# Optimization experiments

Hardware: AMD Instinct MI355X
Metric: run time of the kernel (lower is better)

Reference implementation:

```python
import jax, jax.numpy as jnp
import numpy as np

IN = (16, 16, 16)
OUT = (16, 16, 16)
RT = (8, 8, 8, 8, 8, 8)
RCP = 16
BATCH = 4096


def setup_inputs() -> dict:
    key = jax.random.key(0)
    ks = jax.random.split(key, 14)
    inp = {"x": jax.random.normal(ks[0], (BATCH, int(np.prod(IN))), dtype=jnp.float32)}
    # CP factors of the 6D Tucker core: (rank_tucker_i, rank_cp)
    for i in range(6):
        inp[f"c{i}"] = jax.random.normal(ks[1 + i], (RT[i], RCP), dtype=jnp.float32) * 0.1
    # Tucker factor matrices: out modes then in modes
    dims = list(OUT) + list(IN)
    for i in range(6):
        inp[f"f{i}"] = jax.random.normal(ks[7 + i], (dims[i], RT[i]), dtype=jnp.float32) * 0.1
    inp["bias"] = jnp.zeros((int(np.prod(OUT)),), dtype=jnp.float32)
    return inp


def reference(x, c0, c1, c2, c3, c4, c5, f0, f1, f2, f3, f4, f5, bias):
    # Reconstruct 6D core from its CP factors: (r0,r1,r2,r3,r4,r5)
    core = jnp.einsum('ir,jr,kr,lr,mr,nr->ijklmn', c0, c1, c2, c3, c4, c5)
    # Tucker reconstruction of full weight tensor: (o0,o1,o2,i0,i1,i2)
    W = jnp.einsum('ijklmn,ai,bj,ck,dl,em,fn->abcdef', core, f0, f1, f2, f3, f4, f5)
    x_reshape = x.reshape(-1, *IN)  # (N, i0, i1, i2)
    result = jnp.einsum('abcdef,ndef->nabc', W, x_reshape)  # (N, o0, o1, o2)
    y = result.reshape(-1, int(np.prod(OUT)))
    return y + bias
```

## Files before the change

### kernel.cpp

```cpp
#include <hip/hip_runtime.h>


typedef float f32x4 __attribute__((ext_vector_type(4)));

#define WPB 4

__global__ __launch_bounds__(256, 2)
void kruskal_fused(const float* __restrict__ x,
                   const float* __restrict__ c0, const float* __restrict__ c1,
                   const float* __restrict__ c2, const float* __restrict__ c3,
                   const float* __restrict__ c4, const float* __restrict__ c5,
                   const float* __restrict__ f0, const float* __restrict__ f1,
                   const float* __restrict__ f2, const float* __restrict__ f3,
                   const float* __restrict__ f4, const float* __restrict__ f5,
                   const float* __restrict__ bias,
                   float* __restrict__ out, int N)
{
    __shared__ __align__(16) float g3t[256];
    __shared__ __align__(16) float g4t[256];
    __shared__ __align__(16) float g5t[256];
    __shared__ __align__(16) float g0c[256];
    __shared__ __align__(16) float g1t[256];
    __shared__ __align__(16) float g2t[256];
    __shared__ __align__(16) float bsh[4096];

    const int tid = threadIdx.x;
    {
        const int i = tid >> 4, r = tid & 15;
        float a0 = 0.f, a1 = 0.f, a2 = 0.f, a3 = 0.f, a4 = 0.f, a5 = 0.f;
#pragma unroll
        for (int k = 0; k < 8; ++k) {
            a0 += f0[i * 8 + k] * c0[k * 16 + r];
            a1 += f1[i * 8 + k] * c1[k * 16 + r];
            a2 += f2[i * 8 + k] * c2[k * 16 + r];
            a3 += f3[i * 8 + k] * c3[k * 16 + r];
            a4 += f4[i * 8 + k] * c4[k * 16 + r];
            a5 += f5[i * 8 + k] * c5[k * 16 + r];
        }
        g0c[i * 16 + r] = a0;
        g1t[r * 16 + i] = a1;
        g2t[r * 16 + i] = a2;
        g3t[i * 16 + r] = a3;
        g4t[r * 16 + i] = a4;
        g5t[r * 16 + i] = a5;
    }
    {
        const f32x4* b4 = (const f32x4*)bias;
        f32x4* bs4 = (f32x4*)bsh;
#pragma unroll
        for (int j = 0; j < 4; ++j) bs4[j * 256 + tid] = b4[j * 256 + tid];
    }
    __syncthreads();

    const int lane = tid & 63, waveId = tid >> 6;
    const int eb  = lane >> 2;
    const int fcb = (lane & 3) * 4;

    const int n = blockIdx.x * WPB + waveId;
    if (n >= N) return;
    const float* xn = x + (size_t)n * 4096 + lane * 4;

    f32x4 w1[16];
#pragma unroll
    for (int r = 0; r < 16; ++r) {
        w1[r] = (*(const f32x4*)&g5t[r * 16 + fcb]) * g4t[r * 16 + eb];
        asm volatile("" : "+v"(w1[r]));
    }

    float s[16];
#pragma unroll
    for (int r = 0; r < 16; ++r) s[r] = 0.f;

#define LOAD4(v, dbase)                                                       \
    v##0 = __builtin_nontemporal_load((const f32x4*)(xn + ((dbase) + 0) * 256)); \
    v##1 = __builtin_nontemporal_load((const f32x4*)(xn + ((dbase) + 1) * 256)); \
    v##2 = __builtin_nontemporal_load((const f32x4*)(xn + ((dbase) + 2) * 256)); \
    v##3 = __builtin_nontemporal_load((const f32x4*)(xn + ((dbase) + 3) * 256));

#define COMP1(xv, d)                                                          \
    {                                                                         \
        _Pragma("unroll")                                                     \
        for (int rq = 0; rq < 4; ++rq) {                                      \
            const f32x4 g3q = *(const f32x4*)&g3t[(d) * 16 + rq * 4];         \
            _Pragma("unroll")                                                 \
            for (int rr = 0; rr < 4; ++rr) {                                  \
                const int r = rq * 4 + rr;                                    \
                const float p = w1[r].x * xv.x + w1[r].y * xv.y               \
                              + w1[r].z * xv.z + w1[r].w * xv.w;              \
                s[r] += g3q[rr] * p;                                          \
            }                                                                 \
        }                                                                     \
    }

#define COMP4(v, dbase)                                                       \
    COMP1(v##0, (dbase) + 0) COMP1(v##1, (dbase) + 1)                         \
    COMP1(v##2, (dbase) + 2) COMP1(v##3, (dbase) + 3)

    {
        f32x4 xa0, xa1, xa2, xa3, xb0, xb1, xb2, xb3;
        LOAD4(xa, 0)
        LOAD4(xb, 4)
        COMP4(xa, 0)
        LOAD4(xa, 8)
        COMP4(xb, 4)
        LOAD4(xb, 12)
        COMP4(xa, 8)
        COMP4(xb, 12)
    }
#undef LOAD4
#undef COMP1
#undef COMP4

#pragma unroll
    for (int r = 0; r < 16; ++r) {
        float v = s[r];
        v += __shfl_xor(v, 1, 64);
        v += __shfl_xor(v, 2, 64);
        v += __shfl_xor(v, 4, 64);
        v += __shfl_xor(v, 8, 64);
        v += __shfl_xor(v, 16, 64);
        v += __shfl_xor(v, 32, 64);
        s[r] = v;
    }

    __builtin_amdgcn_sched_barrier(0);

    f32x4 wb[16];
#pragma unroll
    for (int r = 0; r < 16; ++r) {
        wb[r] = (*(const f32x4*)&g2t[r * 16 + fcb]) * g1t[r * 16 + eb];
        asm volatile("" : "+v"(wb[r]));
    }

    float* on = out + (size_t)n * 4096;
#pragma unroll 2
    for (int a = 0; a < 16; ++a) {
        f32x4 acc = *(const f32x4*)&bsh[a * 256 + lane * 4];
#pragma unroll
        for (int rq = 0; rq < 4; ++rq) {
            const f32x4 g0q = *(const f32x4*)&g0c[a * 16 + rq * 4];
#pragma unroll
            for (int rr = 0; rr < 4; ++rr) {
                const int r = rq * 4 + rr;
                acc += (s[r] * g0q[rr]) * wb[r];
            }
        }
        __builtin_nontemporal_store(
            acc, (f32x4*)(on + a * 256 + lane * 4));
    }
}

extern "C" void kernel_launch(void* const* d_in, const int* in_sizes, int n_in,
                              void* d_out, int out_size, void* d_ws, size_t ws_size,
                              hipStream_t stream) {
    const float* x  = (const float*)d_in[0];
    const float* c0 = (const float*)d_in[1];
    const float* c1 = (const float*)d_in[2];
    const float* c2 = (const float*)d_in[3];
    const float* c3 = (const float*)d_in[4];
    const float* c4 = (const float*)d_in[5];
    const float* c5 = (const float*)d_in[6];
    const float* f0 = (const float*)d_in[7];
    const float* f1 = (const float*)d_in[8];
    const float* f2 = (const float*)d_in[9];
    const float* f3 = (const float*)d_in[10];
    const float* f4 = (const float*)d_in[11];
    const float* f5 = (const float*)d_in[12];
    const float* bias = (const float*)d_in[13];
    float* out = (float*)d_out;
    (void)d_ws; (void)ws_size;

    const int N = in_sizes[0] / 4096;
    const int blocks = (N + WPB - 1) / WPB;

    kruskal_fused<<<dim3(blocks), dim3(256), 0, stream>>>(
        x, c0, c1, c2, c3, c4, c5, f0, f1, f2, f3, f4, f5, bias, out, N);
}
```

Measured before the change: 146.8 us.

## Reorder contraction, use transpose-reduce shuffles, premultiply s into output weights

The input phase now accumulates g3-weighted x vectors per rank and applies the g4/g5 weights only once at the end, replacing four multiply-adds per rank per step with one vector FMA. The 16 rank reductions use a recursive-halving transpose-reduce across lanes, which needs far fewer shuffles than 16 separate butterfly trees, and the results are then broadcast back with shuffles. In the output phase s is folded into the per-rank weights, so each step is a single FMA per rank. All three changes aim to cut ALU and cross-lane work. The cost is 64 accumulator registers for t, which may raise register pressure.

```diff
diff --git a/kernel.cpp b/kernel.cpp
--- a/kernel.cpp
+++ b/kernel.cpp
@@ -60,16 +60,9 @@
     if (n >= N) return;
     const float* xn = x + (size_t)n * 4096 + lane * 4;
 
-    f32x4 w1[16];
-#pragma unroll
-    for (int r = 0; r < 16; ++r) {
-        w1[r] = (*(const f32x4*)&g5t[r * 16 + fcb]) * g4t[r * 16 + eb];
-        asm volatile("" : "+v"(w1[r]));
-    }
-
-    float s[16];
-#pragma unroll
-    for (int r = 0; r < 16; ++r) s[r] = 0.f;
+    f32x4 t[16];
+#pragma unroll
+    for (int r = 0; r < 16; ++r) t[r] = f32x4{0.f, 0.f, 0.f, 0.f};
 
 #define LOAD4(v, dbase)                                                       \
     v##0 = __builtin_nontemporal_load((const f32x4*)(xn + ((dbase) + 0) * 256)); \
@@ -83,12 +76,8 @@
         for (int rq = 0; rq < 4; ++rq) {                                      \
             const f32x4 g3q = *(const f32x4*)&g3t[(d) * 16 + rq * 4];         \
             _Pragma("unroll")                                                 \
-            for (int rr = 0; rr < 4; ++rr) {                                  \
-                const int r = rq * 4 + rr;                                    \
-                const float p = w1[r].x * xv.x + w1[r].y * xv.y               \
-                              + w1[r].z * xv.z + w1[r].w * xv.w;              \
-                s[r] += g3q[rr] * p;                                          \
-            }                                                                 \
+            for (int rr = 0; rr < 4; ++rr)                                    \
+                t[rq * 4 + rr] += g3q[rr] * xv;                               \
         }                                                                     \
     }
 
@@ -111,26 +100,67 @@
 #undef COMP1
 #undef COMP4
 
+    float s[16];
 #pragma unroll
     for (int r = 0; r < 16; ++r) {
-        float v = s[r];
-        v += __shfl_xor(v, 1, 64);
-        v += __shfl_xor(v, 2, 64);
-        v += __shfl_xor(v, 4, 64);
-        v += __shfl_xor(v, 8, 64);
-        v += __shfl_xor(v, 16, 64);
-        v += __shfl_xor(v, 32, 64);
-        s[r] = v;
-    }
+        const f32x4 w = (*(const f32x4*)&g5t[r * 16 + fcb]) * g4t[r * 16 + eb];
+        s[r] = w.x * t[r].x + w.y * t[r].y + w.z * t[r].z + w.w * t[r].w;
+    }
+
+    float k8[8];
+    {
+        const bool b = lane & 1;
+#pragma unroll
+        for (int j = 0; j < 8; ++j) {
+            const float snd = b ? s[2 * j] : s[2 * j + 1];
+            const float prt = __shfl_xor(snd, 1, 64);
+            const float kp  = b ? s[2 * j + 1] : s[2 * j];
+            k8[j] = kp + prt;
+        }
+    }
+    float k4[4];
+    {
+        const bool b = (lane >> 1) & 1;
+#pragma unroll
+        for (int j = 0; j < 4; ++j) {
+            const float snd = b ? k8[2 * j] : k8[2 * j + 1];
+            const float prt = __shfl_xor(snd, 2, 64);
+            const float kp  = b ? k8[2 * j + 1] : k8[2 * j];
+            k4[j] = kp + prt;
+        }
+    }
+    float k2[2];
+    {
+        const bool b = (lane >> 2) & 1;
+#pragma unroll
+        for (int j = 0; j < 2; ++j) {
+            const float snd = b ? k4[2 * j] : k4[2 * j + 1];
+            const float prt = __shfl_xor(snd, 4, 64);
+            const float kp  = b ? k4[2 * j + 1] : k4[2 * j];
+            k2[j] = kp + prt;
+        }
+    }
+    float k1;
+    {
+        const bool b = (lane >> 3) & 1;
+        const float snd = b ? k2[0] : k2[1];
+        const float prt = __shfl_xor(snd, 8, 64);
+        const float kp  = b ? k2[1] : k2[0];
+        k1 = kp + prt;
+    }
+    k1 += __shfl_xor(k1, 16, 64);
+    k1 += __shfl_xor(k1, 32, 64);
+    const int gbase = lane & 48;
+#pragma unroll
+    for (int r = 0; r < 16; ++r)
+        s[r] = __shfl(k1, gbase | r, 64);
 
     __builtin_amdgcn_sched_barrier(0);
 
-    f32x4 wb[16];
-#pragma unroll
-    for (int r = 0; r < 16; ++r) {
-        wb[r] = (*(const f32x4*)&g2t[r * 16 + fcb]) * g1t[r * 16 + eb];
-        asm volatile("" : "+v"(wb[r]));
-    }
+    f32x4 sw[16];
+#pragma unroll
+    for (int r = 0; r < 16; ++r)
+        sw[r] = (*(const f32x4*)&g2t[r * 16 + fcb]) * (g1t[r * 16 + eb] * s[r]);
 
     float* on = out + (size_t)n * 4096;
 #pragma unroll 2
@@ -140,10 +170,8 @@
         for (int rq = 0; rq < 4; ++rq) {
             const f32x4 g0q = *(const f32x4*)&g0c[a * 16 + rq * 4];
 #pragma unroll
-            for (int rr = 0; rr < 4; ++rr) {
-                const int r = rq * 4 + rr;
-                acc += (s[r] * g0q[rr]) * wb[r];
-            }
+            for (int rr = 0; rr < 4; ++rr)
+                acc += g0q[rr] * sw[rq * 4 + rr];
         }
         __builtin_nontemporal_store(
             acc, (f32x4*)(on + a * 256 + lane * 4));
```

After: 147.4 us. Within noise of the previous version (+0.4%).
